# Kernel optimization log

Hardware: AMD Instinct MI355X
Metric: run time of the kernel (lower is better)

## Reference

```python
import jax, jax.numpy as jnp
import numpy as np

D = 1024
NUM_HEADS = 16
HEAD_DIM = D // NUM_HEADS
INIT_VALUES = 1e-4


def setup_inputs() -> dict:
    key = jax.random.key(0)
    ks = jax.random.split(key, 24)
    s = 0.02
    inp = {
        "v": jax.random.normal(ks[0], (8, 2048, D), dtype=jnp.float32),
        "l": jax.random.normal(ks[1], (8, 512, D), dtype=jnp.float32),
        "ln_v_g": jnp.ones((D,), jnp.float32),
        "ln_v_b": jnp.zeros((D,), jnp.float32),
        "ln_l_g": jnp.ones((D,), jnp.float32),
        "ln_l_b": jnp.zeros((D,), jnp.float32),
        "gamma_v": jnp.full((D,), INIT_VALUES, jnp.float32),
        "gamma_l": jnp.full((D,), INIT_VALUES, jnp.float32),
    }
    names = ["Wq_v2l", "Wk_v2l", "Wv_v2l", "Wo_v2l", "Wq_l2v", "Wk_l2v", "Wv_l2v", "Wo_l2v"]
    for i, n in enumerate(names):
        inp[n] = jax.random.normal(ks[2 + i], (D, D), dtype=jnp.float32) * s
        inp[n.replace("W", "b")] = jnp.zeros((D,), jnp.float32)
    return inp


def layer_norm(x, g, b, eps=1e-5):
    mu = jnp.mean(x, axis=-1, keepdims=True)
    var = jnp.var(x, axis=-1, keepdims=True)
    return (x - mu) * jax.lax.rsqrt(var + eps) * g + b


def mha(q_in, k_in, v_in, Wq, bq, Wk, bk, Wv, bv, Wo, bo):
    B, Sq, _ = q_in.shape
    Sk = k_in.shape[1]
    # torch Linear: x @ W.T + b
    q = (q_in @ Wq.T + bq).reshape(B, Sq, NUM_HEADS, HEAD_DIM)
    k = (k_in @ Wk.T + bk).reshape(B, Sk, NUM_HEADS, HEAD_DIM)
    v = (v_in @ Wv.T + bv).reshape(B, Sk, NUM_HEADS, HEAD_DIM)
    scores = jnp.einsum("bqhd,bkhd->bhqk", q, k) / np.sqrt(HEAD_DIM).astype(np.float32)
    attn = jax.nn.softmax(scores, axis=-1)
    ctx = jnp.einsum("bhqk,bkhd->bqhd", attn, v).reshape(B, Sq, D)
    return ctx @ Wo.T + bo


def reference(v, l, ln_v_g, ln_v_b, ln_l_g, ln_l_b, gamma_v, gamma_l,
              Wq_v2l, bq_v2l, Wk_v2l, bk_v2l, Wv_v2l, bv_v2l, Wo_v2l, bo_v2l,
              Wq_l2v, bq_l2v, Wk_l2v, bk_l2v, Wv_l2v, bv_l2v, Wo_l2v, bo_l2v):
    # eval mode: dropout and drop_path are identity
    v_norm = layer_norm(v, ln_v_g, ln_v_b)
    l_norm = layer_norm(l, ln_l_g, ln_l_b)
    updated_v = mha(v_norm, l_norm, l_norm,
                    Wq_v2l, bq_v2l, Wk_v2l, bk_v2l, Wv_v2l, bv_v2l, Wo_v2l, bo_v2l)
    updated_l = mha(l_norm, v_norm, v_norm,
                    Wq_l2v, bq_l2v, Wk_l2v, bk_l2v, Wv_l2v, bv_l2v, Wo_l2v, bo_l2v)
    v_out = v + gamma_v * updated_v
    l_out = l + gamma_l * updated_l
    return (v_out, l_out)
```

## Files before the change

kernel.cpp:

```cpp
#include <hip/hip_runtime.h>
#include <hip/hip_bf16.h>
#include <stdint.h>

typedef __bf16 bf16x8 __attribute__((ext_vector_type(8)));
typedef float f32x4 __attribute__((ext_vector_type(4)));
typedef unsigned short u16;

typedef __attribute__((address_space(1))) void as1_void;
typedef __attribute__((address_space(3))) void as3_void;

#define BAR() __builtin_amdgcn_s_barrier()
#define VMCNT(n) asm volatile("s_waitcnt vmcnt(" #n ")" ::: "memory")
#define LGKM0() asm volatile("s_waitcnt lgkmcnt(0)" ::: "memory")

__device__ __forceinline__ u16 f2bf(float f) {
  uint32_t u = __float_as_uint(f);
  u += 0x7fffu + ((u >> 16) & 1u);
  return (u16)(u >> 16);
}

__global__ __launch_bounds__(256) void cvt8_kernel(
    const float4* s0, const float4* s1, const float4* s2, const float4* s3,
    const float4* s4, const float4* s5, const float4* s6, const float4* s7,
    ushort4* d0, ushort4* d1, ushort4* d2, ushort4* d3,
    ushort4* d4, ushort4* d5, ushort4* d6, ushort4* d7) {
  const float4* s; ushort4* d;
  switch (blockIdx.y) {
    case 0: s = s0; d = d0; break;
    case 1: s = s1; d = d1; break;
    case 2: s = s2; d = d2; break;
    case 3: s = s3; d = d3; break;
    case 4: s = s4; d = d4; break;
    case 5: s = s5; d = d5; break;
    case 6: s = s6; d = d6; break;
    default: s = s7; d = d7; break;
  }
  int i = blockIdx.x * 256 + threadIdx.x;
  float4 v = s[i];
  ushort4 o;
  o.x = f2bf(v.x); o.y = f2bf(v.y); o.z = f2bf(v.z); o.w = f2bf(v.w);
  d[i] = o;
}

__global__ __launch_bounds__(256) void ln_kernel(const float* __restrict__ x,
                                                 const float* __restrict__ g,
                                                 const float* __restrict__ b,
                                                 u16* __restrict__ out) {
  int row = blockIdx.x;
  int t = threadIdx.x;
  const float4* xr = (const float4*)(x + (size_t)row * 1024);
  float4 v = xr[t];
  float s = v.x + v.y + v.z + v.w;
  float s2 = v.x * v.x + v.y * v.y + v.z * v.z + v.w * v.w;
#pragma unroll
  for (int off = 1; off < 64; off <<= 1) {
    s += __shfl_xor(s, off);
    s2 += __shfl_xor(s2, off);
  }
  __shared__ float red[8];
  int wv = t >> 6;
  if ((t & 63) == 0) { red[wv] = s; red[4 + wv] = s2; }
  __syncthreads();
  s = red[0] + red[1] + red[2] + red[3];
  s2 = red[4] + red[5] + red[6] + red[7];
  float mu = s * (1.0f / 1024.0f);
  float var = s2 * (1.0f / 1024.0f) - mu * mu;
  float rstd = rsqrtf(var + 1e-5f);
  const float4 gv = ((const float4*)g)[t];
  const float4 bv = ((const float4*)b)[t];
  ushort4 o;
  o.x = f2bf((v.x - mu) * rstd * gv.x + bv.x);
  o.y = f2bf((v.y - mu) * rstd * gv.y + bv.y);
  o.z = f2bf((v.z - mu) * rstd * gv.z + bv.z);
  o.w = f2bf((v.w - mu) * rstd * gv.w + bv.w);
  ((ushort4*)out)[(size_t)row * 256 + t] = o;
}

template <int MODE>
__global__ __launch_bounds__(256) void gemm_kernel(
    const u16* __restrict__ A, const u16* __restrict__ W,
    const float* __restrict__ bias,
    u16* __restrict__ outb, float* __restrict__ outf,
    const float* __restrict__ res, const float* __restrict__ gamma,
    int sk_shift) {
  const int K = 1024, N = 1024;
  int m0 = blockIdx.x * 128, n0 = blockIdx.y * 128;
  int t = threadIdx.x, lane = t & 63, wv = t >> 6;
  int wr = wv >> 1, wc = wv & 1;
  int lr = lane & 15, lk = (lane >> 4) * 8;
  __shared__ u16 As[128 * 32];
  __shared__ u16 Ws[128 * 32];
  f32x4 acc[4][4] = {};
  for (int kt = 0; kt < K / 32; ++kt) {
#pragma unroll
    for (int i = 0; i < 2; ++i) {
      int c = i * 256 + t;
      int row = c >> 2, k8 = (c & 3) << 3;
      const u16* ga = A + (size_t)(m0 + row) * K + kt * 32 + k8;
      const u16* gw = W + (size_t)(n0 + row) * K + kt * 32 + k8;
      __builtin_amdgcn_global_load_lds((const as1_void*)ga, (as3_void*)(As + c * 8), 16, 0, 0);
      __builtin_amdgcn_global_load_lds((const as1_void*)gw, (as3_void*)(Ws + c * 8), 16, 0, 0);
    }
    __syncthreads();
    bf16x8 af[4], wf[4];
#pragma unroll
    for (int m = 0; m < 4; ++m)
      af[m] = *(const bf16x8*)(As + (wr * 64 + m * 16 + lr) * 32 + lk);
#pragma unroll
    for (int n = 0; n < 4; ++n)
      wf[n] = *(const bf16x8*)(Ws + (wc * 64 + n * 16 + lr) * 32 + lk);
#pragma unroll
    for (int m = 0; m < 4; ++m)
#pragma unroll
      for (int n = 0; n < 4; ++n)
        acc[m][n] = __builtin_amdgcn_mfma_f32_16x16x32_bf16(af[m], wf[n], acc[m][n], 0, 0, 0);
    __syncthreads();
  }
  int rowb = m0 + wr * 64 + (lane >> 4) * 4;
#pragma unroll
  for (int m = 0; m < 4; ++m) {
#pragma unroll
    for (int n = 0; n < 4; ++n) {
      int col = n0 + wc * 64 + n * 16 + lr;
      float bcol = bias[col];
#pragma unroll
      for (int r = 0; r < 4; ++r) {
        int row = rowb + m * 16 + r;
        float val = acc[m][n][r] + bcol;
        if (MODE == 0) {
          outb[(size_t)row * N + col] = f2bf(val);
        } else if (MODE == 1) {
          size_t idx = (size_t)row * N + col;
          outf[idx] = res[idx] + gamma[col] * val;
        } else {
          int bb = row >> sk_shift;
          int ss = row & ((1 << sk_shift) - 1);
          int h = col >> 6, d = col & 63;
          outb[((((size_t)bb * 16 + h) * 64 + d) << sk_shift) + ss] = f2bf(val);
        }
      }
    }
  }
}

template <int MODE>
__global__ __launch_bounds__(512, 2) void gemm256_kernel(
    const u16* __restrict__ A, const u16* __restrict__ W,
    const float* __restrict__ bias,
    u16* __restrict__ outb, float* __restrict__ outf,
    const float* __restrict__ res, const float* __restrict__ gamma,
    int mtiles, int sk_shift) {
  const int K = 1024, N = 1024;
  int nwg = mtiles * 4;
  int cpx = nwg >> 3;
  int bid = blockIdx.x;
  int swz = (bid & 7) * cpx + (bid >> 3);
  int mt = swz >> 2, nt = swz & 3;
  int m0 = mt * 256, n0 = nt * 256;

  int t = threadIdx.x, lane = t & 63, wv = t >> 6;
  int wm = wv >> 2, wn = wv & 3;
  int lr = lane & 15, lg = lane >> 4;
  int sa0 = ((lg) ^ (lr & 7)) * 8;
  int sa1 = ((4 + lg) ^ (lr & 7)) * 8;

  __shared__ u16 AB[2][2][256 * 64];
  u16* ldsA0 = &AB[0][0][0];
  u16* ldsB0 = &AB[0][1][0];
  u16* ldsA1 = &AB[1][0][0];
  u16* ldsB1 = &AB[1][1][0];

  int r0 = t >> 3, c0 = t & 7;
  int cs0 = c0 ^ (r0 & 7);
  const u16* gA0 = A + (size_t)(m0 + r0) * K + cs0 * 8;
  const u16* gA1 = gA0 + (size_t)64 * K;
  const u16* gB0 = W + (size_t)(n0 + r0) * K + cs0 * 8;
  const u16* gB1 = gB0 + (size_t)64 * K;

  auto STG = [&](u16* ldsbase, const u16* g0, const u16* g1, int half, int kt) {
    __builtin_amdgcn_global_load_lds(
        (const as1_void*)(g0 + (size_t)half * 128 * K + kt * 64),
        (as3_void*)(ldsbase + (half * 128 + r0) * 64 + c0 * 8), 16, 0, 0);
    __builtin_amdgcn_global_load_lds(
        (const as1_void*)(g1 + (size_t)half * 128 * K + kt * 64),
        (as3_void*)(ldsbase + (half * 128 + r0 + 64) * 64 + c0 * 8), 16, 0, 0);
  };

  f32x4 acc[8][4] = {};
  bf16x8 aX[4][2], bX[2][2], bY[2][2];

  auto LD_A = [&](const u16* base, int mo) {
#pragma unroll
    for (int m = 0; m < 4; ++m) {
      const u16* rp = base + (wm * 128 + (mo + m) * 16 + lr) * 64;
      aX[m][0] = *(const bf16x8*)(rp + sa0);
      aX[m][1] = *(const bf16x8*)(rp + sa1);
    }
  };
  auto LD_B = [&](bf16x8 (&dst)[2][2], const u16* base, int no) {
#pragma unroll
    for (int n = 0; n < 2; ++n) {
      const u16* rp = base + (wn * 64 + (no + n) * 16 + lr) * 64;
      dst[n][0] = *(const bf16x8*)(rp + sa0);
      dst[n][1] = *(const bf16x8*)(rp + sa1);
    }
  };
  auto QD = [&](bf16x8 (&bf)[2][2], int mo, int no) {
#pragma unroll
    for (int m = 0; m < 4; ++m)
#pragma unroll
      for (int n = 0; n < 2; ++n) {
        acc[mo + m][no + n] = __builtin_amdgcn_mfma_f32_16x16x32_bf16(
            aX[m][0], bf[n][0], acc[mo + m][no + n], 0, 0, 0);
        acc[mo + m][no + n] = __builtin_amdgcn_mfma_f32_16x16x32_bf16(
            aX[m][1], bf[n][1], acc[mo + m][no + n], 0, 0, 0);
      }
  };

  STG(ldsA0, gA0, gA1, 0, 0); STG(ldsA0, gA0, gA1, 1, 0);
  STG(ldsB0, gB0, gB1, 0, 0); STG(ldsB0, gB0, gB1, 1, 0);
  STG(ldsA1, gA0, gA1, 0, 1); STG(ldsA1, gA0, gA1, 1, 1);
  STG(ldsB1, gB0, gB1, 0, 1); STG(ldsB1, gB0, gB1, 1, 1);
  VMCNT(8);
  BAR();

  const int NIT = K / 128;
#pragma unroll 1
  for (int it = 0; it < NIT; ++it) {
    bool st = (it + 1 < NIT);
    int ktA = 2 * it;
    LD_A(ldsA0, 0); LD_B(bX, ldsB0, 0);
    BAR(); LGKM0();
    __builtin_amdgcn_s_setprio(1); QD(bX, 0, 0); __builtin_amdgcn_s_setprio(0);
    BAR();
    LD_B(bY, ldsB0, 2);
    BAR(); LGKM0();
    __builtin_amdgcn_s_setprio(1); QD(bY, 0, 2); __builtin_amdgcn_s_setprio(0);
    BAR();
    LD_A(ldsA0, 4);
    if (st) { STG(ldsB0, gB0, gB1, 0, ktA + 2); STG(ldsB0, gB0, gB1, 1, ktA + 2); }
    BAR(); LGKM0();
    __builtin_amdgcn_s_setprio(1); QD(bY, 4, 2); __builtin_amdgcn_s_setprio(0);
    BAR();
    if (st) { STG(ldsA0, gA0, gA1, 0, ktA + 2); STG(ldsA0, gA0, gA1, 1, ktA + 2); }
    if (st) { VMCNT(8); } else { VMCNT(0); }
    BAR();
    __builtin_amdgcn_s_setprio(1); QD(bX, 4, 0); __builtin_amdgcn_s_setprio(0);
    BAR();
    LD_A(ldsA1, 0); LD_B(bX, ldsB1, 0);
    BAR(); LGKM0();
    __builtin_amdgcn_s_setprio(1); QD(bX, 0, 0); __builtin_amdgcn_s_setprio(0);
    BAR();
    LD_B(bY, ldsB1, 2);
    BAR(); LGKM0();
    __builtin_amdgcn_s_setprio(1); QD(bY, 0, 2); __builtin_amdgcn_s_setprio(0);
    BAR();
    LD_A(ldsA1, 4);
    if (st) { STG(ldsB1, gB0, gB1, 0, ktA + 3); STG(ldsB1, gB0, gB1, 1, ktA + 3); }
    BAR(); LGKM0();
    __builtin_amdgcn_s_setprio(1); QD(bY, 4, 2); __builtin_amdgcn_s_setprio(0);
    BAR();
    if (st) { STG(ldsA1, gA0, gA1, 0, ktA + 3); STG(ldsA1, gA0, gA1, 1, ktA + 3); }
    if (st) { VMCNT(8); }
    BAR();
    __builtin_amdgcn_s_setprio(1); QD(bX, 4, 0); __builtin_amdgcn_s_setprio(0);
    BAR();
  }

  int rowb = m0 + wm * 128 + lg * 4;
#pragma unroll
  for (int mi = 0; mi < 8; ++mi) {
#pragma unroll
    for (int n = 0; n < 4; ++n) {
      int col = n0 + wn * 64 + n * 16 + lr;
      float bcol = bias[col];
#pragma unroll
      for (int r = 0; r < 4; ++r) {
        int row = rowb + mi * 16 + r;
        float val = acc[mi][n][r] + bcol;
        if (MODE == 0) {
          outb[(size_t)row * N + col] = f2bf(val);
        } else if (MODE == 1) {
          size_t idx = (size_t)row * N + col;
          outf[idx] = res[idx] + gamma[col] * val;
        } else {
          int bb = row >> sk_shift;
          int ss = row & ((1 << sk_shift) - 1);
          int h = col >> 6, d = col & 63;
          outb[((((size_t)bb * 16 + h) * 64 + d) << sk_shift) + ss] = f2bf(val);
        }
      }
    }
  }
}

__global__ __launch_bounds__(512) void attn_kernel(
    const u16* __restrict__ Q, const u16* __restrict__ Kmat,
    const u16* __restrict__ Vt, u16* __restrict__ ctx,
    int Sq, int Sk, int nq_shift) {
  int f = blockIdx.x;
  int xcd = f & 7, slot = f >> 3;
  int group = xcd * 16 + (slot >> nq_shift);
  int qt = slot & ((1 << nq_shift) - 1);
  int b = group >> 4, h = group & 15;
  int t = threadIdx.x, lane = t & 63, wv = t >> 6;
  int lr = lane & 15, lg = lane >> 4;

  __shared__ u16 Ks[2][64 * 64];
  __shared__ u16 Vs[2][64 * 64];
  __shared__ u16 Pl[8][16 * 64];
  u16* pw = Pl[wv];

  const u16* Qb = Q + ((size_t)(b * Sq + qt * 128 + wv * 16)) * 1024 + h * 64;
  bf16x8 qf0 = *(const bf16x8*)(Qb + (size_t)lr * 1024 + lg * 8);
  bf16x8 qf1 = *(const bf16x8*)(Qb + (size_t)lr * 1024 + 32 + lg * 8);
  const u16* Kb = Kmat + (size_t)(b * Sk) * 1024 + h * 64;
  const u16* Vb = Vt + ((size_t)(b * 16 + h)) * 64 * Sk;

  int trow = t >> 3, tblk = t & 7;
  int srcoff = ((tblk ^ (trow & 7)) * 8);
  const u16* gk = Kb + (size_t)trow * 1024 + srcoff;
  const u16* gv = Vb + (size_t)trow * Sk + srcoff;

  __builtin_amdgcn_global_load_lds((const as1_void*)gk, (as3_void*)(Ks[0] + t * 8), 16, 0, 0);
  __builtin_amdgcn_global_load_lds((const as1_void*)gv, (as3_void*)(Vs[0] + t * 8), 16, 0, 0);
  __syncthreads();

  float m_run[4] = {-1e30f, -1e30f, -1e30f, -1e30f};
  float l_run[4] = {0.f, 0.f, 0.f, 0.f};
  f32x4 accO[4] = {};
  int nt = Sk >> 6;
  for (int kt = 0; kt < nt; ++kt) {
    int cur = kt & 1;
    if (kt + 1 < nt) {
      const u16* gk2 = gk + (size_t)(kt + 1) * 64 * 1024;
      const u16* gv2 = gv + (size_t)(kt + 1) * 64;
      __builtin_amdgcn_global_load_lds((const as1_void*)gk2, (as3_void*)(Ks[cur ^ 1] + t * 8), 16, 0, 0);
      __builtin_amdgcn_global_load_lds((const as1_void*)gv2, (as3_void*)(Vs[cur ^ 1] + t * 8), 16, 0, 0);
    }
    f32x4 s[4] = {};
    __builtin_amdgcn_s_setprio(1);
#pragma unroll
    for (int n = 0; n < 4; ++n) {
      int row = n * 16 + lr;
      const u16* kp = Ks[cur] + row * 64;
      int sw = row & 7;
      bf16x8 kf0 = *(const bf16x8*)(kp + ((lg ^ sw) * 8));
      bf16x8 kf1 = *(const bf16x8*)(kp + (((4 + lg) ^ sw) * 8));
      s[n] = __builtin_amdgcn_mfma_f32_16x16x32_bf16(qf0, kf0, s[n], 0, 0, 0);
      s[n] = __builtin_amdgcn_mfma_f32_16x16x32_bf16(qf1, kf1, s[n], 0, 0, 0);
    }
    __builtin_amdgcn_s_setprio(0);
    float fac[4];
    float pr[4][4];
#pragma unroll
    for (int r = 0; r < 4; ++r) {
      float mx = fmaxf(fmaxf(s[0][r], s[1][r]), fmaxf(s[2][r], s[3][r]));
      mx = fmaxf(mx, __shfl_xor(mx, 1));
      mx = fmaxf(mx, __shfl_xor(mx, 2));
      mx = fmaxf(mx, __shfl_xor(mx, 4));
      mx = fmaxf(mx, __shfl_xor(mx, 8));
      float mnew = fmaxf(m_run[r], mx * 0.125f);
      float sum = 0.f;
#pragma unroll
      for (int n = 0; n < 4; ++n) {
        float p = __expf(s[n][r] * 0.125f - mnew);
        pr[n][r] = p;
        sum += p;
      }
      sum += __shfl_xor(sum, 1);
      sum += __shfl_xor(sum, 2);
      sum += __shfl_xor(sum, 4);
      sum += __shfl_xor(sum, 8);
      float ff = __expf(m_run[r] - mnew);
      l_run[r] = l_run[r] * ff + sum;
      m_run[r] = mnew;
      fac[r] = ff;
    }
#pragma unroll
    for (int n = 0; n < 4; ++n)
#pragma unroll
      for (int r = 0; r < 4; ++r)
        accO[n][r] *= fac[r];
#pragma unroll
    for (int n = 0; n < 4; ++n)
#pragma unroll
      for (int r = 0; r < 4; ++r) {
        int row2 = lg * 4 + r;
        int col = n * 16 + lr;
        int idx = row2 * 64 + (((((col >> 3) ^ (row2 & 7))) << 3) | (col & 7));
        pw[idx] = f2bf(pr[n][r]);
      }
    __builtin_amdgcn_s_setprio(1);
#pragma unroll
    for (int kk = 0; kk < 2; ++kk) {
      int pb = (kk * 4 + lg) ^ (lr & 7);
      bf16x8 pf = *(const bf16x8*)(pw + lr * 64 + pb * 8);
#pragma unroll
      for (int n = 0; n < 4; ++n) {
        int row = n * 16 + lr;
        int vb = (kk * 4 + lg) ^ (row & 7);
        bf16x8 vf = *(const bf16x8*)(Vs[cur] + row * 64 + vb * 8);
        accO[n] = __builtin_amdgcn_mfma_f32_16x16x32_bf16(pf, vf, accO[n], 0, 0, 0);
      }
    }
    __builtin_amdgcn_s_setprio(0);
    __syncthreads();
  }
  u16* cb = ctx + ((size_t)(b * Sq + qt * 128 + wv * 16)) * 1024 + h * 64;
#pragma unroll
  for (int n = 0; n < 4; ++n) {
#pragma unroll
    for (int r = 0; r < 4; ++r) {
      float o = accO[n][r] * (1.0f / l_run[r]);
      cb[(size_t)(lg * 4 + r) * 1024 + n * 16 + lr] = f2bf(o);
    }
  }
}

extern "C" void kernel_launch(void* const* d_in, const int* in_sizes, int n_in,
                              void* d_out, int out_size, void* d_ws, size_t ws_size,
                              hipStream_t stream) {
  const float* v = (const float*)d_in[0];
  const float* l = (const float*)d_in[1];
  const float* ln_v_g = (const float*)d_in[2];
  const float* ln_v_b = (const float*)d_in[3];
  const float* ln_l_g = (const float*)d_in[4];
  const float* ln_l_b = (const float*)d_in[5];
  const float* gamma_v = (const float*)d_in[6];
  const float* gamma_l = (const float*)d_in[7];
  const float* Wf[8];
  const float* Bf[8];
  for (int i = 0; i < 8; ++i) {
    Wf[i] = (const float*)d_in[8 + 2 * i];
    Bf[i] = (const float*)d_in[9 + 2 * i];
  }
  float* v_out = (float*)d_out;
  float* l_out = v_out + (size_t)16384 * 1024;

  char* p = (char*)d_ws;
  auto alloc = [&](size_t bytes) {
    char* r = p;
    p += (bytes + 255) & ~(size_t)255;
    return r;
  };
  u16* Wbf[8];
  for (int i = 0; i < 8; ++i) Wbf[i] = (u16*)alloc((size_t)1024 * 1024 * 2);
  u16* vn   = (u16*)alloc((size_t)16384 * 1024 * 2);
  u16* lnm  = (u16*)alloc((size_t)4096 * 1024 * 2);
  u16* bufA = (u16*)alloc((size_t)16384 * 1024 * 2);
  u16* bufB = (u16*)alloc((size_t)4096 * 1024 * 2);
  u16* bufC = (u16*)alloc((size_t)4096 * 1024 * 2);
  u16* bufD = (u16*)alloc((size_t)16384 * 1024 * 2);

  cvt8_kernel<<<dim3(1024, 8), 256, 0, stream>>>(
      (const float4*)Wf[0], (const float4*)Wf[1], (const float4*)Wf[2], (const float4*)Wf[3],
      (const float4*)Wf[4], (const float4*)Wf[5], (const float4*)Wf[6], (const float4*)Wf[7],
      (ushort4*)Wbf[0], (ushort4*)Wbf[1], (ushort4*)Wbf[2], (ushort4*)Wbf[3],
      (ushort4*)Wbf[4], (ushort4*)Wbf[5], (ushort4*)Wbf[6], (ushort4*)Wbf[7]);
  ln_kernel<<<16384, 256, 0, stream>>>(v, ln_v_g, ln_v_b, vn);
  ln_kernel<<<4096, 256, 0, stream>>>(l, ln_l_g, ln_l_b, lnm);

  dim3 blk(256);
  dim3 blk512(512);
  gemm256_kernel<0><<<dim3(256), blk512, 0, stream>>>(vn, Wbf[0], Bf[0], bufA, nullptr, nullptr, nullptr, 64, 0);
  gemm_kernel<0><<<dim3(32, 8), blk, 0, stream>>>(lnm, Wbf[1], Bf[1], bufB, nullptr, nullptr, nullptr, 0);
  gemm_kernel<2><<<dim3(32, 8), blk, 0, stream>>>(lnm, Wbf[2], Bf[2], bufC, nullptr, nullptr, nullptr, 9);
  attn_kernel<<<dim3(2048), blk512, 0, stream>>>(bufA, bufB, bufC, bufD, 2048, 512, 4);
  gemm256_kernel<1><<<dim3(256), blk512, 0, stream>>>(bufD, Wbf[3], Bf[3], nullptr, v_out, v, gamma_v, 64, 0);
  gemm_kernel<0><<<dim3(32, 8), blk, 0, stream>>>(lnm, Wbf[4], Bf[4], bufB, nullptr, nullptr, nullptr, 0);
  gemm256_kernel<0><<<dim3(256), blk512, 0, stream>>>(vn, Wbf[5], Bf[5], bufA, nullptr, nullptr, nullptr, 64, 0);
  gemm256_kernel<2><<<dim3(256), blk512, 0, stream>>>(vn, Wbf[6], Bf[6], bufD, nullptr, nullptr, nullptr, 64, 11);
  attn_kernel<<<dim3(512), blk512, 0, stream>>>(bufB, bufA, bufD, bufC, 512, 2048, 2);
  gemm_kernel<1><<<dim3(32, 8), blk, 0, stream>>>(bufC, Wbf[7], Bf[7], nullptr, l_out, l, gamma_l, 0);
}
```

Before: 519.9 us.

## Rewrite attention with 32x32 MFMA, register-resident P, and folded softmax scale

The attention kernel is rewritten to use 32x32x16 bf16 MFMAs with 32 query rows per wave and 256-thread blocks. K and V fragments are read straight from global memory instead of being staged through double-buffered LDS. P stays in registers via packed bf16 conversion and permlane32 swaps rather than a round trip through LDS. The softmax scale and log2(e) are folded into the Q projection GEMM epilogue so exp2 can be used, and rescaling is skipped unless the running max grows by more than a threshold. This removes LDS traffic, barriers and shuffle reductions, at the cost of uncoalesced direct global loads with no explicit prefetch and reliance on cache reuse across waves.

```diff
diff --git a/kernel.cpp b/kernel.cpp
--- a/kernel.cpp
+++ b/kernel.cpp
@@ -4,6 +4,8 @@
 
 typedef __bf16 bf16x8 __attribute__((ext_vector_type(8)));
 typedef float f32x4 __attribute__((ext_vector_type(4)));
+typedef float f32x16 __attribute__((ext_vector_type(16)));
+typedef uint32_t u32x4 __attribute__((ext_vector_type(4)));
 typedef unsigned short u16;
 
 typedef __attribute__((address_space(1))) void as1_void;
@@ -17,6 +19,12 @@
   uint32_t u = __float_as_uint(f);
   u += 0x7fffu + ((u >> 16) & 1u);
   return (u16)(u >> 16);
+}
+
+__device__ __forceinline__ uint32_t cvtpk(float lo, float hi) {
+  uint32_t r;
+  asm("v_cvt_pk_bf16_f32 %0, %1, %2" : "=v"(r) : "v"(lo), "v"(hi));
+  return r;
 }
 
 __global__ __launch_bounds__(256) void cvt8_kernel(
@@ -82,7 +90,7 @@
     const float* __restrict__ bias,
     u16* __restrict__ outb, float* __restrict__ outf,
     const float* __restrict__ res, const float* __restrict__ gamma,
-    int sk_shift) {
+    int sk_shift, float ascale) {
   const int K = 1024, N = 1024;
   int m0 = blockIdx.x * 128, n0 = blockIdx.y * 128;
   int t = threadIdx.x, lane = t & 63, wv = t >> 6;
@@ -126,7 +134,7 @@
 #pragma unroll
       for (int r = 0; r < 4; ++r) {
         int row = rowb + m * 16 + r;
-        float val = acc[m][n][r] + bcol;
+        float val = (acc[m][n][r] + bcol) * ascale;
         if (MODE == 0) {
           outb[(size_t)row * N + col] = f2bf(val);
         } else if (MODE == 1) {
@@ -149,7 +157,7 @@
     const float* __restrict__ bias,
     u16* __restrict__ outb, float* __restrict__ outf,
     const float* __restrict__ res, const float* __restrict__ gamma,
-    int mtiles, int sk_shift) {
+    int mtiles, int sk_shift, float ascale) {
   const int K = 1024, N = 1024;
   int nwg = mtiles * 4;
   int cpx = nwg >> 3;
@@ -277,7 +285,7 @@
 #pragma unroll
       for (int r = 0; r < 4; ++r) {
         int row = rowb + mi * 16 + r;
-        float val = acc[mi][n][r] + bcol;
+        float val = (acc[mi][n][r] + bcol) * ascale;
         if (MODE == 0) {
           outb[(size_t)row * N + col] = f2bf(val);
         } else if (MODE == 1) {
@@ -294,7 +302,7 @@
   }
 }
 
-__global__ __launch_bounds__(512) void attn_kernel(
+__global__ __launch_bounds__(256, 4) void attn_kernel(
     const u16* __restrict__ Q, const u16* __restrict__ Kmat,
     const u16* __restrict__ Vt, u16* __restrict__ ctx,
     int Sq, int Sk, int nq_shift) {
@@ -304,117 +312,89 @@
   int qt = slot & ((1 << nq_shift) - 1);
   int b = group >> 4, h = group & 15;
   int t = threadIdx.x, lane = t & 63, wv = t >> 6;
-  int lr = lane & 15, lg = lane >> 4;
-
-  __shared__ u16 Ks[2][64 * 64];
-  __shared__ u16 Vs[2][64 * 64];
-  __shared__ u16 Pl[8][16 * 64];
-  u16* pw = Pl[wv];
-
-  const u16* Qb = Q + ((size_t)(b * Sq + qt * 128 + wv * 16)) * 1024 + h * 64;
-  bf16x8 qf0 = *(const bf16x8*)(Qb + (size_t)lr * 1024 + lg * 8);
-  bf16x8 qf1 = *(const bf16x8*)(Qb + (size_t)lr * 1024 + 32 + lg * 8);
-  const u16* Kb = Kmat + (size_t)(b * Sk) * 1024 + h * 64;
-  const u16* Vb = Vt + ((size_t)(b * 16 + h)) * 64 * Sk;
-
-  int trow = t >> 3, tblk = t & 7;
-  int srcoff = ((tblk ^ (trow & 7)) * 8);
-  const u16* gk = Kb + (size_t)trow * 1024 + srcoff;
-  const u16* gv = Vb + (size_t)trow * Sk + srcoff;
-
-  __builtin_amdgcn_global_load_lds((const as1_void*)gk, (as3_void*)(Ks[0] + t * 8), 16, 0, 0);
-  __builtin_amdgcn_global_load_lds((const as1_void*)gv, (as3_void*)(Vs[0] + t * 8), 16, 0, 0);
-  __syncthreads();
-
-  float m_run[4] = {-1e30f, -1e30f, -1e30f, -1e30f};
-  float l_run[4] = {0.f, 0.f, 0.f, 0.f};
-  f32x4 accO[4] = {};
-  int nt = Sk >> 6;
+  int l31 = lane & 31, hi = lane >> 5;
+
+  int q0 = qt * 128 + wv * 32;
+  const u16* Qb = Q + (size_t)(b * Sq + q0 + l31) * 1024 + h * 64 + hi * 8;
+  bf16x8 qf[4];
+#pragma unroll
+  for (int ds = 0; ds < 4; ++ds) qf[ds] = *(const bf16x8*)(Qb + ds * 16);
+
+  const u16* Kb = Kmat + (size_t)(b * Sk + l31) * 1024 + h * 64 + hi * 8;
+  const u16* Vb0 = Vt + (size_t)((b * 16 + h) * 64 + l31) * Sk + hi * 8;
+  const u16* Vb1 = Vb0 + (size_t)32 * Sk;
+
+  f32x16 acc0 = {}, acc1 = {};
+  float m_run = -1e30f, l_run = 0.f;
+
+  int nt = Sk >> 5;
   for (int kt = 0; kt < nt; ++kt) {
-    int cur = kt & 1;
-    if (kt + 1 < nt) {
-      const u16* gk2 = gk + (size_t)(kt + 1) * 64 * 1024;
-      const u16* gv2 = gv + (size_t)(kt + 1) * 64;
-      __builtin_amdgcn_global_load_lds((const as1_void*)gk2, (as3_void*)(Ks[cur ^ 1] + t * 8), 16, 0, 0);
-      __builtin_amdgcn_global_load_lds((const as1_void*)gv2, (as3_void*)(Vs[cur ^ 1] + t * 8), 16, 0, 0);
-    }
-    f32x4 s[4] = {};
-    __builtin_amdgcn_s_setprio(1);
-#pragma unroll
-    for (int n = 0; n < 4; ++n) {
-      int row = n * 16 + lr;
-      const u16* kp = Ks[cur] + row * 64;
-      int sw = row & 7;
-      bf16x8 kf0 = *(const bf16x8*)(kp + ((lg ^ sw) * 8));
-      bf16x8 kf1 = *(const bf16x8*)(kp + (((4 + lg) ^ sw) * 8));
-      s[n] = __builtin_amdgcn_mfma_f32_16x16x32_bf16(qf0, kf0, s[n], 0, 0, 0);
-      s[n] = __builtin_amdgcn_mfma_f32_16x16x32_bf16(qf1, kf1, s[n], 0, 0, 0);
-    }
-    __builtin_amdgcn_s_setprio(0);
-    float fac[4];
-    float pr[4][4];
-#pragma unroll
-    for (int r = 0; r < 4; ++r) {
-      float mx = fmaxf(fmaxf(s[0][r], s[1][r]), fmaxf(s[2][r], s[3][r]));
-      mx = fmaxf(mx, __shfl_xor(mx, 1));
-      mx = fmaxf(mx, __shfl_xor(mx, 2));
-      mx = fmaxf(mx, __shfl_xor(mx, 4));
-      mx = fmaxf(mx, __shfl_xor(mx, 8));
-      float mnew = fmaxf(m_run[r], mx * 0.125f);
-      float sum = 0.f;
-#pragma unroll
-      for (int n = 0; n < 4; ++n) {
-        float p = __expf(s[n][r] * 0.125f - mnew);
-        pr[n][r] = p;
-        sum += p;
+    const u16* kp = Kb + (size_t)(kt * 32) * 1024;
+    f32x16 s = {};
+#pragma unroll
+    for (int ds = 0; ds < 4; ++ds) {
+      bf16x8 ka = *(const bf16x8*)(kp + ds * 16);
+      s = __builtin_amdgcn_mfma_f32_32x32x16_bf16(ka, qf[ds], s, 0, 0, 0);
+    }
+    bf16x8 vf0[2], vf1[2];
+#pragma unroll
+    for (int ks = 0; ks < 2; ++ks) {
+      vf0[ks] = *(const bf16x8*)(Vb0 + kt * 32 + ks * 16);
+      vf1[ks] = *(const bf16x8*)(Vb1 + kt * 32 + ks * 16);
+    }
+    float mx = s[0];
+#pragma unroll
+    for (int i = 1; i < 16; ++i) mx = fmaxf(mx, s[i]);
+    mx = fmaxf(mx, __shfl_xor(mx, 32));
+    if (__any(mx > m_run + 8.f)) {
+      float mnew = fmaxf(m_run, mx);
+      float fac = __builtin_amdgcn_exp2f(m_run - mnew);
+#pragma unroll
+      for (int r = 0; r < 16; ++r) {
+        int src = (r & 3) + 8 * (r >> 2) + 4 * hi;
+        float fr = __shfl(fac, src);
+        acc0[r] *= fr;
+        acc1[r] *= fr;
       }
-      sum += __shfl_xor(sum, 1);
-      sum += __shfl_xor(sum, 2);
-      sum += __shfl_xor(sum, 4);
-      sum += __shfl_xor(sum, 8);
-      float ff = __expf(m_run[r] - mnew);
-      l_run[r] = l_run[r] * ff + sum;
-      m_run[r] = mnew;
-      fac[r] = ff;
-    }
-#pragma unroll
-    for (int n = 0; n < 4; ++n)
-#pragma unroll
-      for (int r = 0; r < 4; ++r)
-        accO[n][r] *= fac[r];
-#pragma unroll
-    for (int n = 0; n < 4; ++n)
-#pragma unroll
-      for (int r = 0; r < 4; ++r) {
-        int row2 = lg * 4 + r;
-        int col = n * 16 + lr;
-        int idx = row2 * 64 + (((((col >> 3) ^ (row2 & 7))) << 3) | (col & 7));
-        pw[idx] = f2bf(pr[n][r]);
-      }
-    __builtin_amdgcn_s_setprio(1);
-#pragma unroll
-    for (int kk = 0; kk < 2; ++kk) {
-      int pb = (kk * 4 + lg) ^ (lr & 7);
-      bf16x8 pf = *(const bf16x8*)(pw + lr * 64 + pb * 8);
-#pragma unroll
-      for (int n = 0; n < 4; ++n) {
-        int row = n * 16 + lr;
-        int vb = (kk * 4 + lg) ^ (row & 7);
-        bf16x8 vf = *(const bf16x8*)(Vs[cur] + row * 64 + vb * 8);
-        accO[n] = __builtin_amdgcn_mfma_f32_16x16x32_bf16(pf, vf, accO[n], 0, 0, 0);
-      }
-    }
-    __builtin_amdgcn_s_setprio(0);
-    __syncthreads();
-  }
-  u16* cb = ctx + ((size_t)(b * Sq + qt * 128 + wv * 16)) * 1024 + h * 64;
-#pragma unroll
-  for (int n = 0; n < 4; ++n) {
-#pragma unroll
-    for (int r = 0; r < 4; ++r) {
-      float o = accO[n][r] * (1.0f / l_run[r]);
-      cb[(size_t)(lg * 4 + r) * 1024 + n * 16 + lr] = f2bf(o);
-    }
+      l_run *= fac;
+      m_run = mnew;
+    }
+    float sum = 0.f;
+#pragma unroll
+    for (int i = 0; i < 16; ++i) {
+      s[i] = __builtin_amdgcn_exp2f(s[i] - m_run);
+      sum += s[i];
+    }
+    sum += __shfl_xor(sum, 32);
+    l_run += sum;
+    bf16x8 pa[2];
+#pragma unroll
+    for (int half = 0; half < 2; ++half) {
+      int o = half * 8;
+      uint32_t a0 = cvtpk(s[o + 0], s[o + 1]);
+      uint32_t a1 = cvtpk(s[o + 2], s[o + 3]);
+      uint32_t b0 = cvtpk(s[o + 4], s[o + 5]);
+      uint32_t b1 = cvtpk(s[o + 6], s[o + 7]);
+      asm("v_permlane32_swap_b32 %0, %1" : "+v"(a0), "+v"(b0));
+      asm("v_permlane32_swap_b32 %0, %1" : "+v"(a1), "+v"(b1));
+      u32x4 w;
+      w[0] = a0; w[1] = a1; w[2] = b0; w[3] = b1;
+      pa[half] = __builtin_bit_cast(bf16x8, w);
+    }
+#pragma unroll
+    for (int ks = 0; ks < 2; ++ks) {
+      acc0 = __builtin_amdgcn_mfma_f32_32x32x16_bf16(pa[ks], vf0[ks], acc0, 0, 0, 0);
+      acc1 = __builtin_amdgcn_mfma_f32_32x32x16_bf16(pa[ks], vf1[ks], acc1, 0, 0, 0);
+    }
+  }
+  float linv = 1.0f / l_run;
+  u16* cb = ctx + (size_t)(b * Sq + q0) * 1024 + h * 64;
+#pragma unroll
+  for (int r = 0; r < 16; ++r) {
+    int src = (r & 3) + 8 * (r >> 2) + 4 * hi;
+    float li = __shfl(linv, src);
+    cb[(size_t)src * 1024 + l31] = f2bf(acc0[r] * li);
+    cb[(size_t)src * 1024 + 32 + l31] = f2bf(acc1[r] * li);
   }
 }
 
@@ -453,6 +433,8 @@
   u16* bufC = (u16*)alloc((size_t)4096 * 1024 * 2);
   u16* bufD = (u16*)alloc((size_t)16384 * 1024 * 2);
 
+  const float QSC = 0.125f * 1.4426950408889634f;
+
   cvt8_kernel<<<dim3(1024, 8), 256, 0, stream>>>(
       (const float4*)Wf[0], (const float4*)Wf[1], (const float4*)Wf[2], (const float4*)Wf[3],
       (const float4*)Wf[4], (const float4*)Wf[5], (const float4*)Wf[6], (const float4*)Wf[7],
@@ -463,14 +445,14 @@
 
   dim3 blk(256);
   dim3 blk512(512);
-  gemm256_kernel<0><<<dim3(256), blk512, 0, stream>>>(vn, Wbf[0], Bf[0], bufA, nullptr, nullptr, nullptr, 64, 0);
-  gemm_kernel<0><<<dim3(32, 8), blk, 0, stream>>>(lnm, Wbf[1], Bf[1], bufB, nullptr, nullptr, nullptr, 0);
-  gemm_kernel<2><<<dim3(32, 8), blk, 0, stream>>>(lnm, Wbf[2], Bf[2], bufC, nullptr, nullptr, nullptr, 9);
-  attn_kernel<<<dim3(2048), blk512, 0, stream>>>(bufA, bufB, bufC, bufD, 2048, 512, 4);
-  gemm256_kernel<1><<<dim3(256), blk512, 0, stream>>>(bufD, Wbf[3], Bf[3], nullptr, v_out, v, gamma_v, 64, 0);
-  gemm_kernel<0><<<dim3(32, 8), blk, 0, stream>>>(lnm, Wbf[4], Bf[4], bufB, nullptr, nullptr, nullptr, 0);
-  gemm256_kernel<0><<<dim3(256), blk512, 0, stream>>>(vn, Wbf[5], Bf[5], bufA, nullptr, nullptr, nullptr, 64, 0);
-  gemm256_kernel<2><<<dim3(256), blk512, 0, stream>>>(vn, Wbf[6], Bf[6], bufD, nullptr, nullptr, nullptr, 64, 11);
-  attn_kernel<<<dim3(512), blk512, 0, stream>>>(bufB, bufA, bufD, bufC, 512, 2048, 2);
-  gemm_kernel<1><<<dim3(32, 8), blk, 0, stream>>>(bufC, Wbf[7], Bf[7], nullptr, l_out, l, gamma_l, 0);
-}
+  gemm256_kernel<0><<<dim3(256), blk512, 0, stream>>>(vn, Wbf[0], Bf[0], bufA, nullptr, nullptr, nullptr, 64, 0, QSC);
+  gemm_kernel<0><<<dim3(32, 8), blk, 0, stream>>>(lnm, Wbf[1], Bf[1], bufB, nullptr, nullptr, nullptr, 0, 1.0f);
+  gemm_kernel<2><<<dim3(32, 8), blk, 0, stream>>>(lnm, Wbf[2], Bf[2], bufC, nullptr, nullptr, nullptr, 9, 1.0f);
+  attn_kernel<<<dim3(2048), blk, 0, stream>>>(bufA, bufB, bufC, bufD, 2048, 512, 4);
+  gemm256_kernel<1><<<dim3(256), blk512, 0, stream>>>(bufD, Wbf[3], Bf[3], nullptr, v_out, v, gamma_v, 64, 0, 1.0f);
+  gemm_kernel<0><<<dim3(32, 8), blk, 0, stream>>>(lnm, Wbf[4], Bf[4], bufB, nullptr, nullptr, nullptr, 0, QSC);
+  gemm256_kernel<0><<<dim3(256), blk512, 0, stream>>>(vn, Wbf[5], Bf[5], bufA, nullptr, nullptr, nullptr, 64, 0, 1.0f);
+  gemm256_kernel<2><<<dim3(256), blk512, 0, stream>>>(vn, Wbf[6], Bf[6], bufD, nullptr, nullptr, nullptr, 64, 11, 1.0f);
+  attn_kernel<<<dim3(512), blk, 0, stream>>>(bufB, bufA, bufD, bufC, 512, 2048, 2);
+  gemm_kernel<1><<<dim3(32, 8), blk, 0, stream>>>(bufC, Wbf[7], Bf[7], nullptr, l_out, l, gamma_l, 0, 1.0f);
+}
```

Result: slower. 573.4 us (+10.3%).
